# Optimization experiments

Hardware: AMD Instinct MI355X
Metric: run time of the kernel (lower is better)

The kernel has to match this reference:

```python
import jax, jax.numpy as jnp
import numpy as np

B, T = 2048, 8
IN_DIM, OUT_DIM, E = 1024, 4096, 12


def setup_inputs() -> dict:
    key = jax.random.key(0)
    k = jax.random.split(key, 6)
    s = 1.0 / np.sqrt(IN_DIM)
    sg = 1.0 / np.sqrt(OUT_DIM)
    return {
        "x": jax.random.normal(k[0], (B, 1, IN_DIM), dtype=jnp.float32),
        "t": jax.random.normal(k[1], (B, T, OUT_DIM), dtype=jnp.float32),
        "W": jax.random.uniform(k[2], (E, IN_DIM, OUT_DIM), dtype=jnp.float32, minval=-s, maxval=s),
        "b": jax.random.uniform(k[3], (E, OUT_DIM), dtype=jnp.float32, minval=-s, maxval=s),
        "Wg": jax.random.uniform(k[4], (OUT_DIM, E), dtype=jnp.float32, minval=-sg, maxval=sg),
        "bg": jax.random.uniform(k[5], (E,), dtype=jnp.float32, minval=-sg, maxval=sg),
    }


def reference(x, t, W, b, Wg, bg):
    # x: [B,1,in], t: [B,T,out], W: [E,in,out], b: [E,out], Wg: [out,E], bg: [E]
    x_flat = x[:, 0, :]                                   # [B,in]
    t_mean = t.mean(axis=1)                               # [B,out]
    gate_logits = t_mean @ Wg + bg                        # [B,E]
    top1 = jnp.argmax(gate_logits, axis=-1)               # [B]
    # Dense per-expert linear, then select the top-1 expert's row per token.
    all_out = jnp.einsum('bi,eio->beo', x_flat, W) + b    # [B,E,out]
    out = all_out[jnp.arange(x.shape[0]), top1]           # [B,out]
    return out[:, None, :]                                # [B,1,out]
```

## Files before the change

### kernel.cpp

```cpp
#include <hip/hip_runtime.h>
#include <hip/hip_bf16.h>

#define B_ROWS  2048
#define T_DIM   8
#define IN_DIM  1024
#define OUT_DIM 4096
#define NE      12

#define M_TILE 128
#define N_TILE 128
#define K_STEP 32
#define NSTEP  (IN_DIM / K_STEP)

typedef __attribute__((ext_vector_type(8))) short short8;
typedef __attribute__((ext_vector_type(4))) float f32x4;

union S8U { short8 s; unsigned u[4]; };

__device__ __forceinline__ unsigned cvt2(float a, float b) {
  __hip_bfloat162 h = __float22bfloat162_rn(make_float2(a, b));
  union { __hip_bfloat162 h; unsigned u; } c; c.h = h;
  return c.u;
}

__device__ __forceinline__ void barrier_lgkm() {
  asm volatile("s_waitcnt lgkmcnt(0)" ::: "memory");
  __builtin_amdgcn_s_barrier();
}

__global__ __launch_bounds__(256) void wg_transpose(
    const float* __restrict__ Wg, float* __restrict__ wgt)
{
  const int c = blockIdx.x * 256 + threadIdx.x;
  #pragma unroll
  for (int e = 0; e < NE; ++e)
    wgt[(size_t)e * OUT_DIM + c] = Wg[(size_t)c * NE + e];
}

__global__ __launch_bounds__(256) void gate_kernel(
    const float* __restrict__ t, const float* __restrict__ wgt,
    const float* __restrict__ bg, int* __restrict__ counts,
    int* __restrict__ rowlist)
{
  const int b   = blockIdx.x;
  const int tid = threadIdx.x;
  const float* tb = t + (size_t)b * T_DIM * OUT_DIM;

  float4 m[4];
  #pragma unroll
  for (int it = 0; it < 4; ++it) {
    const int c = (tid + it * 256) * 4;
    float4 s = make_float4(0.f, 0.f, 0.f, 0.f);
    #pragma unroll
    for (int tt = 0; tt < T_DIM; ++tt) {
      const float4 v = *(const float4*)(tb + (size_t)tt * OUT_DIM + c);
      s.x += v.x; s.y += v.y; s.z += v.z; s.w += v.w;
    }
    m[it] = make_float4(s.x * 0.125f, s.y * 0.125f, s.z * 0.125f, s.w * 0.125f);
  }

  float part[NE];
  #pragma unroll
  for (int e = 0; e < NE; ++e) {
    float acc = 0.f;
    #pragma unroll
    for (int it = 0; it < 4; ++it) {
      const int c = (tid + it * 256) * 4;
      const float4 w = *(const float4*)(wgt + (size_t)e * OUT_DIM + c);
      acc += m[it].x * w.x; acc += m[it].y * w.y;
      acc += m[it].z * w.z; acc += m[it].w * w.w;
    }
    part[e] = acc;
  }

  double d[NE];
  #pragma unroll
  for (int e = 0; e < NE; ++e) d[e] = (double)part[e];
  #pragma unroll
  for (int off = 32; off > 0; off >>= 1) {
    #pragma unroll
    for (int e = 0; e < NE; ++e) d[e] += __shfl_down(d[e], off, 64);
  }

  __shared__ double wsred[4][NE];
  const int lane = tid & 63, wave = tid >> 6;
  if (lane == 0) {
    #pragma unroll
    for (int e = 0; e < NE; ++e) wsred[wave][e] = d[e];
  }
  __syncthreads();

  if (tid == 0) {
    double best = -1e300; int bi = 0;
    #pragma unroll
    for (int e = 0; e < NE; ++e) {
      const double v = wsred[0][e] + wsred[1][e] + wsred[2][e] + wsred[3][e] + (double)bg[e];
      if (v > best) { best = v; bi = e; }
    }
    const int pos = atomicAdd(&counts[bi], 1);
    rowlist[bi * B_ROWS + pos] = b;
  }
}

__global__ __launch_bounds__(256) void gate_fallback(
    const float* __restrict__ t, const float* __restrict__ Wg,
    const float* __restrict__ bg, int* __restrict__ counts,
    int* __restrict__ rowlist)
{
  const int b   = blockIdx.x;
  const int tid = threadIdx.x;
  const float* tb = t + (size_t)b * T_DIM * OUT_DIM;

  float part[NE];
  #pragma unroll
  for (int e = 0; e < NE; ++e) part[e] = 0.f;
  #pragma unroll
  for (int it = 0; it < 4; ++it) {
    const int c = (tid + it * 256) * 4;
    float4 s = make_float4(0.f, 0.f, 0.f, 0.f);
    #pragma unroll
    for (int tt = 0; tt < T_DIM; ++tt) {
      const float4 v = *(const float4*)(tb + (size_t)tt * OUT_DIM + c);
      s.x += v.x; s.y += v.y; s.z += v.z; s.w += v.w;
    }
    const float mm[4] = { s.x * 0.125f, s.y * 0.125f, s.z * 0.125f, s.w * 0.125f };
    #pragma unroll
    for (int j = 0; j < 4; ++j) {
      const float* wg = Wg + (size_t)(c + j) * NE;
      #pragma unroll
      for (int e = 0; e < NE; ++e) part[e] += mm[j] * wg[e];
    }
  }
  double d[NE];
  #pragma unroll
  for (int e = 0; e < NE; ++e) d[e] = (double)part[e];
  #pragma unroll
  for (int off = 32; off > 0; off >>= 1) {
    #pragma unroll
    for (int e = 0; e < NE; ++e) d[e] += __shfl_down(d[e], off, 64);
  }
  __shared__ double wsred[4][NE];
  const int lane = tid & 63, wave = tid >> 6;
  if (lane == 0) {
    #pragma unroll
    for (int e = 0; e < NE; ++e) wsred[wave][e] = d[e];
  }
  __syncthreads();
  if (tid == 0) {
    double best = -1e300; int bi = 0;
    #pragma unroll
    for (int e = 0; e < NE; ++e) {
      const double v = wsred[0][e] + wsred[1][e] + wsred[2][e] + wsred[3][e] + (double)bg[e];
      if (v > best) { best = v; bi = e; }
    }
    const int pos = atomicAdd(&counts[bi], 1);
    rowlist[bi * B_ROWS + pos] = b;
  }
}

__global__ __launch_bounds__(256) void expert_gemm(
    const float* __restrict__ x, const float* __restrict__ W,
    const float* __restrict__ bias, const int* __restrict__ counts,
    const int* __restrict__ rowlist, float* __restrict__ out)
{
  const int e    = blockIdx.z;
  const int cnt  = counts[e];
  const int row0 = blockIdx.y * M_TILE;
  if (row0 >= cnt) return;
  const int c0   = blockIdx.x * N_TILE;
  const int* rl  = rowlist + e * B_ROWS;

  __shared__ short8 xa[2][512];
  __shared__ short8 wb[2][512];

  const int tid  = threadIdx.x;
  const int lane = tid & 63;
  const int wave = tid >> 6;

  const int sg  = (tid >> 4) & 3;
  const int slr = tid & 15;
  const int smb = tid >> 6;

  int arow0, arow1;
  {
    const int g0 = row0 + smb * 16 + slr;
    const int g1 = row0 + (smb + 4) * 16 + slr;
    arow0 = rl[g0 < cnt ? g0 : cnt - 1];
    arow1 = rl[g1 < cnt ? g1 : cnt - 1];
  }
  const float* xp0 = x + (size_t)arow0 * IN_DIM + sg * 8;
  const float* xp1 = x + (size_t)arow1 * IN_DIM + sg * 8;
  const float* wp  = W + (size_t)e * IN_DIM * OUT_DIM
                       + (size_t)(sg * 8) * OUT_DIM + c0 + smb * 16 + slr;

  const int wm = (wave >> 1) * 64;
  const int wn = (wave & 1) * 64;
  const int abase = (wave >> 1) * 256;
  const int bbase = (wave & 1) * 256;

  f32x4 acc[4][4];
  #pragma unroll
  for (int m = 0; m < 4; ++m)
    #pragma unroll
    for (int n = 0; n < 4; ++n)
      #pragma unroll
      for (int q = 0; q < 4; ++q) acc[m][n][q] = 0.f;

  float4 a0lo, a0hi, a1lo, a1hi;
  float w0[8], w1[8];

#define ISSUE_LOADS(K)                                                  \
  {                                                                     \
    a0lo = *(const float4*)(xp0 + (K));                                 \
    a0hi = *(const float4*)(xp0 + (K) + 4);                             \
    a1lo = *(const float4*)(xp1 + (K));                                 \
    a1hi = *(const float4*)(xp1 + (K) + 4);                             \
    const float* p = wp + (size_t)(K) * OUT_DIM;                        \
    _Pragma("unroll")                                                   \
    for (int j = 0; j < 8; ++j) {                                       \
      w0[j] = p[(size_t)j * OUT_DIM];                                   \
      w1[j] = p[(size_t)j * OUT_DIM + 64];                              \
    }                                                                   \
  }

  ISSUE_LOADS(0);

  for (int it = 0; it < NSTEP; ++it) {
    S8U av0, av1, bv0, bv1;
    av0.u[0] = cvt2(a0lo.x, a0lo.y); av0.u[1] = cvt2(a0lo.z, a0lo.w);
    av0.u[2] = cvt2(a0hi.x, a0hi.y); av0.u[3] = cvt2(a0hi.z, a0hi.w);
    av1.u[0] = cvt2(a1lo.x, a1lo.y); av1.u[1] = cvt2(a1lo.z, a1lo.w);
    av1.u[2] = cvt2(a1hi.x, a1hi.y); av1.u[3] = cvt2(a1hi.z, a1hi.w);
    #pragma unroll
    for (int q = 0; q < 4; ++q) {
      bv0.u[q] = cvt2(w0[2 * q], w0[2 * q + 1]);
      bv1.u[q] = cvt2(w1[2 * q], w1[2 * q + 1]);
    }

    if (it + 1 < NSTEP) ISSUE_LOADS((it + 1) * K_STEP);

    const int buf = it & 1;
    xa[buf][tid]       = av0.s;
    xa[buf][tid + 256] = av1.s;
    wb[buf][tid]       = bv0.s;
    wb[buf][tid + 256] = bv1.s;
    barrier_lgkm();

    short8 af[4], bf[4];
    #pragma unroll
    for (int m = 0; m < 4; ++m) af[m] = xa[buf][abase + m * 64 + lane];
    #pragma unroll
    for (int n = 0; n < 4; ++n) bf[n] = wb[buf][bbase + n * 64 + lane];
    #pragma unroll
    for (int m = 0; m < 4; ++m)
      #pragma unroll
      for (int n = 0; n < 4; ++n)
        acc[m][n] = __builtin_amdgcn_mfma_f32_16x16x32_bf16(af[m], bf[n], acc[m][n], 0, 0, 0);
  }
#undef ISSUE_LOADS

  const int lr = lane & 15;
  const int lq = (lane >> 4) * 4;
  float bcol[4];
  #pragma unroll
  for (int n = 0; n < 4; ++n)
    bcol[n] = bias[e * OUT_DIM + c0 + wn + n * 16 + lr];

  #pragma unroll
  for (int m = 0; m < 4; ++m) {
    #pragma unroll
    for (int r = 0; r < 4; ++r) {
      const int gidx = row0 + wm + m * 16 + lq + r;
      if (gidx >= cnt) continue;
      const int grow = rl[gidx];
      float* orow = out + (size_t)grow * OUT_DIM;
      #pragma unroll
      for (int n = 0; n < 4; ++n) {
        const int col = c0 + wn + n * 16 + lr;
        orow[col] = acc[m][n][r] + bcol[n];
      }
    }
  }
}

extern "C" void kernel_launch(void* const* d_in, const int* in_sizes, int n_in,
                              void* d_out, int out_size, void* d_ws, size_t ws_size,
                              hipStream_t stream) {
  (void)in_sizes; (void)n_in; (void)out_size;
  const float* x  = (const float*)d_in[0];
  const float* t  = (const float*)d_in[1];
  const float* W  = (const float*)d_in[2];
  const float* bb = (const float*)d_in[3];
  const float* Wg = (const float*)d_in[4];
  const float* bg = (const float*)d_in[5];
  float* out = (float*)d_out;

  int*   counts  = (int*)d_ws;
  int*   rowlist = (int*)d_ws + 16;
  float* wgt     = (float*)((char*)d_ws + 64 + NE * B_ROWS * 4);
  const size_t need = 64 + (size_t)NE * B_ROWS * 4 + (size_t)NE * OUT_DIM * 4;

  hipMemsetAsync(counts, 0, 16 * sizeof(int), stream);
  if (ws_size >= need) {
    wg_transpose<<<OUT_DIM / 256, 256, 0, stream>>>(Wg, wgt);
    gate_kernel<<<B_ROWS, 256, 0, stream>>>(t, wgt, bg, counts, rowlist);
  } else {
    gate_fallback<<<B_ROWS, 256, 0, stream>>>(t, Wg, bg, counts, rowlist);
  }

  dim3 grid(OUT_DIM / N_TILE, (B_ROWS + M_TILE - 1) / M_TILE, NE);
  expert_gemm<<<grid, 256, 0, stream>>>(x, W, bb, counts, rowlist, out);
}
```

Before: 172.2 us.

## Prepack gathered x rows to bf16 and stream them via direct global-to-LDS loads

```diff
diff --git a/kernel.cpp b/kernel.cpp
--- a/kernel.cpp
+++ b/kernel.cpp
@@ -11,6 +11,7 @@
 #define N_TILE 128
 #define K_STEP 32
 #define NSTEP  (IN_DIM / K_STEP)
+#define PACK_TILES 2
 
 typedef __attribute__((ext_vector_type(8))) short short8;
 typedef __attribute__((ext_vector_type(4))) float f32x4;
@@ -26,6 +27,12 @@
 __device__ __forceinline__ void barrier_lgkm() {
   asm volatile("s_waitcnt lgkmcnt(0)" ::: "memory");
   __builtin_amdgcn_s_barrier();
+}
+
+__device__ __forceinline__ void gload_lds16(const void* g, void* l) {
+  __builtin_amdgcn_global_load_lds(
+      (const __attribute__((address_space(1))) void*)g,
+      (__attribute__((address_space(3))) void*)l, 16, 0, 0);
 }
 
 __global__ __launch_bounds__(256) void wg_transpose(
@@ -158,10 +165,42 @@
   }
 }
 
-__global__ __launch_bounds__(256) void expert_gemm(
-    const float* __restrict__ x, const float* __restrict__ W,
-    const float* __restrict__ bias, const int* __restrict__ counts,
-    const int* __restrict__ rowlist, float* __restrict__ out)
+__global__ __launch_bounds__(256) void pack_x(
+    const float* __restrict__ x, const int* __restrict__ counts,
+    const int* __restrict__ rowlist, short8* __restrict__ pxa)
+{
+  const int e   = blockIdx.x;
+  const int rt  = blockIdx.y;
+  const int it  = blockIdx.z;
+  const int cnt = counts[e];
+  const int row0 = rt * M_TILE;
+  if (row0 >= cnt) return;
+  const int* rl = rowlist + e * B_ROWS;
+  const int tid = threadIdx.x;
+  const int sg = (tid >> 4) & 3, slr = tid & 15, smb = tid >> 6;
+
+  int g0 = row0 + smb * 16 + slr;        g0 = g0 < cnt ? g0 : cnt - 1;
+  int g1 = row0 + (smb + 4) * 16 + slr;  g1 = g1 < cnt ? g1 : cnt - 1;
+  const float* xp0 = x + (size_t)rl[g0] * IN_DIM + sg * 8 + it * K_STEP;
+  const float* xp1 = x + (size_t)rl[g1] * IN_DIM + sg * 8 + it * K_STEP;
+
+  const float4 a = *(const float4*)xp0, b = *(const float4*)(xp0 + 4);
+  const float4 c = *(const float4*)xp1, d = *(const float4*)(xp1 + 4);
+  S8U v0, v1;
+  v0.u[0] = cvt2(a.x, a.y); v0.u[1] = cvt2(a.z, a.w);
+  v0.u[2] = cvt2(b.x, b.y); v0.u[3] = cvt2(b.z, b.w);
+  v1.u[0] = cvt2(c.x, c.y); v1.u[1] = cvt2(c.z, c.w);
+  v1.u[2] = cvt2(d.x, d.y); v1.u[3] = cvt2(d.z, d.w);
+
+  short8* dst = pxa + ((size_t)(e * PACK_TILES + rt) * NSTEP + it) * 512;
+  dst[tid]       = v0.s;
+  dst[tid + 256] = v1.s;
+}
+
+__global__ __launch_bounds__(256) void expert_gemm_packed(
+    const float* __restrict__ W, const float* __restrict__ bias,
+    const int* __restrict__ counts, const int* __restrict__ rowlist,
+    const short8* __restrict__ pxa, float* __restrict__ out)
 {
   const int e    = blockIdx.z;
   const int cnt  = counts[e];
@@ -176,7 +215,121 @@
   const int tid  = threadIdx.x;
   const int lane = tid & 63;
   const int wave = tid >> 6;
-
+  const int sg = (tid >> 4) & 3, slr = tid & 15, smb = tid >> 6;
+
+  const float* wp = W + (size_t)e * IN_DIM * OUT_DIM
+                      + (size_t)(sg * 8) * OUT_DIM + c0 + smb * 16 + slr;
+
+  const short8* at = pxa + (size_t)(e * PACK_TILES + blockIdx.y) * NSTEP * 512
+                   + wave * 128 + lane;
+
+  const int wm = (wave >> 1) * 64, wn = (wave & 1) * 64;
+  const int abase = (wave >> 1) * 256, bbase = (wave & 1) * 256;
+
+  f32x4 acc[4][4];
+  #pragma unroll
+  for (int m = 0; m < 4; ++m)
+    #pragma unroll
+    for (int n = 0; n < 4; ++n)
+      #pragma unroll
+      for (int q = 0; q < 4; ++q) acc[m][n][q] = 0.f;
+
+  float w0[8], w1[8];
+
+#define W_ISSUE(K)                                                      \
+  {                                                                     \
+    const float* p = wp + (size_t)(K) * OUT_DIM;                        \
+    _Pragma("unroll")                                                   \
+    for (int j = 0; j < 8; ++j) {                                       \
+      w0[j] = p[(size_t)j * OUT_DIM];                                   \
+      w1[j] = p[(size_t)j * OUT_DIM + 64];                              \
+    }                                                                   \
+  }
+
+  W_ISSUE(0);
+  gload_lds16(at,      &xa[0][wave * 128]);
+  gload_lds16(at + 64, &xa[0][wave * 128 + 64]);
+  __builtin_amdgcn_sched_barrier(0);
+
+  #pragma unroll 2
+  for (int it = 0; it < NSTEP; ++it) {
+    const int buf = it & 1;
+
+    S8U bv0, bv1;
+    #pragma unroll
+    for (int q = 0; q < 4; ++q) {
+      bv0.u[q] = cvt2(w0[2 * q], w0[2 * q + 1]);
+      bv1.u[q] = cvt2(w1[2 * q], w1[2 * q + 1]);
+    }
+
+    const int itn = (it + 1 < NSTEP) ? it + 1 : 0;
+    W_ISSUE(itn * K_STEP);
+
+    wb[buf][tid]       = bv0.s;
+    wb[buf][tid + 256] = bv1.s;
+
+    asm volatile("s_waitcnt vmcnt(16) lgkmcnt(0)" ::: "memory");
+    __builtin_amdgcn_s_barrier();
+
+    gload_lds16(at + (size_t)itn * 512,      &xa[buf ^ 1][wave * 128]);
+    gload_lds16(at + (size_t)itn * 512 + 64, &xa[buf ^ 1][wave * 128 + 64]);
+    __builtin_amdgcn_sched_barrier(0);
+
+    short8 af[4], bf[4];
+    #pragma unroll
+    for (int m = 0; m < 4; ++m) af[m] = xa[buf][abase + m * 64 + lane];
+    #pragma unroll
+    for (int n = 0; n < 4; ++n) bf[n] = wb[buf][bbase + n * 64 + lane];
+    #pragma unroll
+    for (int m = 0; m < 4; ++m)
+      #pragma unroll
+      for (int n = 0; n < 4; ++n)
+        acc[m][n] = __builtin_amdgcn_mfma_f32_16x16x32_bf16(af[m], bf[n], acc[m][n], 0, 0, 0);
+  }
+#undef W_ISSUE
+
+  const int lr = lane & 15;
+  const int lq = (lane >> 4) * 4;
+  float bcol[4];
+  #pragma unroll
+  for (int n = 0; n < 4; ++n)
+    bcol[n] = bias[e * OUT_DIM + c0 + wn + n * 16 + lr];
+
+  #pragma unroll
+  for (int m = 0; m < 4; ++m) {
+    #pragma unroll
+    for (int r = 0; r < 4; ++r) {
+      const int gidx = row0 + wm + m * 16 + lq + r;
+      if (gidx >= cnt) continue;
+      const int grow = rl[gidx];
+      float* orow = out + (size_t)grow * OUT_DIM;
+      #pragma unroll
+      for (int n = 0; n < 4; ++n) {
+        const int col = c0 + wn + n * 16 + lr;
+        orow[col] = acc[m][n][r] + bcol[n];
+      }
+    }
+  }
+}
+
+__global__ __launch_bounds__(256) void expert_gemm_legacy(
+    const float* __restrict__ x, const float* __restrict__ W,
+    const float* __restrict__ bias, const int* __restrict__ counts,
+    const int* __restrict__ rowlist, float* __restrict__ out, int y_off)
+{
+  const int e    = blockIdx.z;
+  const int cnt  = counts[e];
+  const int row0 = (blockIdx.y + y_off) * M_TILE;
+  if (row0 >= cnt) return;
+  const int c0   = blockIdx.x * N_TILE;
+  const int* rl  = rowlist + e * B_ROWS;
+
+  __shared__ short8 xa[2][512];
+  __shared__ short8 wb[2][512];
+
+  const int tid  = threadIdx.x;
+  const int lane = tid & 63;
+  const int wave = tid >> 6;
   const int sg  = (tid >> 4) & 3;
   const int slr = tid & 15;
   const int smb = tid >> 6;
@@ -295,19 +448,30 @@
   const float* bg = (const float*)d_in[5];
   float* out = (float*)d_out;
 
-  int*   counts  = (int*)d_ws;
-  int*   rowlist = (int*)d_ws + 16;
-  float* wgt     = (float*)((char*)d_ws + 64 + NE * B_ROWS * 4);
-  const size_t need = 64 + (size_t)NE * B_ROWS * 4 + (size_t)NE * OUT_DIM * 4;
-
-  hipMemsetAsync(counts, 0, 16 * sizeof(int), stream);
-  if (ws_size >= need) {
+  char*  base    = (char*)d_ws;
+  int*   counts  = (int*)base;
+  int*   rowlist = (int*)(base + 64);
+  float* wgt     = (float*)(base + 98368);
+  short8* pxa    = (short8*)(base + 295936);
+  const size_t need_wgt  = 98368 + 196608;
+  const size_t need_pack = 295936 + (size_t)NE * PACK_TILES * NSTEP * 512 * 16;
+
+  hipMemsetAsync(counts, 0, 64, stream);
+  if (ws_size >= need_wgt) {
     wg_transpose<<<OUT_DIM / 256, 256, 0, stream>>>(Wg, wgt);
     gate_kernel<<<B_ROWS, 256, 0, stream>>>(t, wgt, bg, counts, rowlist);
   } else {
     gate_fallback<<<B_ROWS, 256, 0, stream>>>(t, Wg, bg, counts, rowlist);
   }
 
-  dim3 grid(OUT_DIM / N_TILE, (B_ROWS + M_TILE - 1) / M_TILE, NE);
-  expert_gemm<<<grid, 256, 0, stream>>>(x, W, bb, counts, rowlist, out);
-}
+  if (ws_size >= need_pack) {
+    pack_x<<<dim3(NE, PACK_TILES, NSTEP), 256, 0, stream>>>(x, counts, rowlist, pxa);
+    expert_gemm_packed<<<dim3(OUT_DIM / N_TILE, PACK_TILES, NE), 256, 0, stream>>>(
+        W, bb, counts, rowlist, pxa, out);
+    expert_gemm_legacy<<<dim3(OUT_DIM / N_TILE, B_ROWS / M_TILE - PACK_TILES, NE),
+                         256, 0, stream>>>(x, W, bb, counts, rowlist, out, PACK_TILES);
+  } else {
+    expert_gemm_legacy<<<dim3(OUT_DIM / N_TILE, B_ROWS / M_TILE, NE),
+                         256, 0, stream>>>(x, W, bb, counts, rowlist, out, 0);
+  }
+}
```

Result: faster. 163.2 us (-5.3%).
